# Performance work log

Hardware: AMD Instinct MI355X
Metric: run time of the kernel (lower is better)

## Reference

```python
import jax, jax.numpy as jnp
import numpy as np

DIM = 1024
NUM_HEADS = 16
HEAD_DIM = DIM // NUM_HEADS
SCALE = 1.0 / HEAD_DIM  # NOTE: module uses 1/head_dim, not 1/sqrt(head_dim)


def setup_inputs() -> dict:
    key = jax.random.key(0)
    ks = jax.random.split(key, 9)
    B, S = 2, 2048
    init = lambda k, shape: jax.random.normal(k, shape, dtype=jnp.float32) * 0.02
    return {
        "x": jax.random.normal(ks[0], (B, S, DIM), dtype=jnp.float32),
        "wq": init(ks[1], (DIM, DIM)), "bq": jnp.zeros((DIM,), jnp.float32),
        "wk": init(ks[2], (DIM, DIM)), "bk": jnp.zeros((DIM,), jnp.float32),
        "wv": init(ks[3], (DIM, DIM)), "bv": jnp.zeros((DIM,), jnp.float32),
        "wo": init(ks[4], (DIM, DIM)), "bo": jnp.zeros((DIM,), jnp.float32),
    }


def _attn(x, wq, bq, wk, bk, wv, bv, wo, bo):
    B, S, D = x.shape
    H, hd = NUM_HEADS, HEAD_DIM
    # projections; weights stored as (in, out) so y = x @ w + b
    q = (x @ wq + bq).reshape(B, S, H, hd).transpose(0, 2, 1, 3)  # [B,H,S,hd]
    k = (x @ wk + bk).reshape(B, S, H, hd).transpose(0, 2, 1, 3)
    v = (x @ wv + bv).reshape(B, S, H, hd).transpose(0, 2, 1, 3)
    scores = jnp.einsum("bhqd,bhkd->bhqk", q, k) * SCALE  # [B,H,S,S]
    # Module's mask: triu(ones, diagonal=0) kept -> attends to positions j >= i
    i = jnp.arange(S)[:, None]
    j = jnp.arange(S)[None, :]
    allowed = j >= i  # [S,S]
    scores = jnp.where(allowed[None, None], scores, -jnp.inf)
    probs = jax.nn.softmax(scores, axis=-1)
    # dropout is identity in eval/reference mode
    out = jnp.einsum("bhqk,bhkd->bhqd", probs, v)  # [B,H,S,hd]
    out = out.transpose(0, 2, 1, 3).reshape(B, S, D)
    return out @ wo + bo


def reference(x, wq, bq, wk, bk, wv, bv, wo, bo):
    return _attn(x, wq, bq, wk, bk, wv, bv, wo, bo)
```

## Files before the change

kernel.cpp:

```cpp
#include <hip/hip_runtime.h>
#include <hip/hip_bf16.h>


constexpr int NH    = 16;
constexpr int HD    = 64;
constexpr int BATCH = 2;
constexpr int SEQ   = 2048;
constexpr int DIMSZ = 1024;
constexpr float SCALE = 1.0f / 64.0f;
constexpr float QSCL = SCALE * 1.44269504088896f;

typedef __attribute__((ext_vector_type(8))) short short8;
typedef __attribute__((ext_vector_type(4))) float f32x4;
typedef __attribute__((ext_vector_type(4))) unsigned short ushort4v;

__device__ inline unsigned short f2bf(float f) {
    __hip_bfloat16 h = __float2bfloat16(f);
    unsigned short u;
    __builtin_memcpy(&u, &h, 2);
    return u;
}

__device__ __forceinline__ void gload_lds16(const void* g, void* l) {
    __builtin_amdgcn_global_load_lds(
        (const __attribute__((address_space(1))) unsigned int*)g,
        (__attribute__((address_space(3))) unsigned int*)l, 16, 0, 0);
}

__global__ __launch_bounds__(256) void cvt_x(const float* __restrict__ src,
                                             unsigned short* __restrict__ dst)
{
    const int i = blockIdx.x * 256 + threadIdx.x;
    const float4* s4 = reinterpret_cast<const float4*>(src);
    const float4 a = s4[(size_t)i * 2];
    const float4 b = s4[(size_t)i * 2 + 1];
    short8 o;
    o[0] = (short)f2bf(a.x); o[1] = (short)f2bf(a.y);
    o[2] = (short)f2bf(a.z); o[3] = (short)f2bf(a.w);
    o[4] = (short)f2bf(b.x); o[5] = (short)f2bf(b.y);
    o[6] = (short)f2bf(b.z); o[7] = (short)f2bf(b.w);
    *reinterpret_cast<short8*>(&dst[(size_t)i * 8]) = o;
}

__global__ __launch_bounds__(256) void cvt_w(const float* __restrict__ wq,
                                             const float* __restrict__ wk,
                                             const float* __restrict__ wv,
                                             const float* __restrict__ wo,
                                             unsigned short* __restrict__ wt)
{
    __shared__ float tile[64][65];
    const int t = threadIdx.x;
    const float* src = (blockIdx.z == 0) ? wq : (blockIdx.z == 1) ? wk
                     : (blockIdx.z == 2) ? wv : wo;
    const int n0 = blockIdx.x * 64, k0 = blockIdx.y * 64;

#pragma unroll
    for (int r = 0; r < 64; r += 16) {
        const int row = r + (t >> 4);
        const int c4 = (t & 15) * 4;
        const float4 v = *reinterpret_cast<const float4*>(
            &src[(size_t)(k0 + row) * DIMSZ + n0 + c4]);
        tile[row][c4 + 0] = v.x;
        tile[row][c4 + 1] = v.y;
        tile[row][c4 + 2] = v.z;
        tile[row][c4 + 3] = v.w;
    }
    __syncthreads();
#pragma unroll
    for (int rr = 0; rr < 2; ++rr) {
        const int n = rr * 32 + (t >> 3);
        const int kk0 = (t & 7) * 8;
        short8 pk;
#pragma unroll
        for (int e = 0; e < 8; ++e)
            pk[e] = (short)f2bf(tile[kk0 + e][n]);
        *reinterpret_cast<short8*>(
            &wt[((size_t)blockIdx.z * DIMSZ + n0 + n) * DIMSZ + k0 + kk0]) = pk;
    }
}

template <int EPI>
__global__ __launch_bounds__(256, 2) void mfma_gemm(
    const unsigned short* __restrict__ A, const unsigned short* __restrict__ Bt,
    const float* __restrict__ b0, const float* __restrict__ b1,
    const float* __restrict__ b2,
    unsigned short* __restrict__ q_o, unsigned short* __restrict__ k_o,
    unsigned short* __restrict__ vt_o, float* __restrict__ c_out)
{
    __shared__ unsigned short As[2][128 * 64];
    __shared__ unsigned short Bs[2][128 * 64];

    const int tid = threadIdx.x;
    const int lane = tid & 63;
    const int wv_ = tid >> 6;
    const int wr = wv_ >> 1, wc = wv_ & 1;
    const int c = lane & 15, g = lane >> 4;
    const int m0 = blockIdx.y * 128;
    const int nb0 = blockIdx.x * 128;
    const int wbase = (tid & 192) * 8;
    const int lrow = tid >> 3, ld0 = (tid & 7) * 8;

    f32x4 acc[4][4];
#pragma unroll
    for (int i = 0; i < 4; ++i)
#pragma unroll
        for (int j = 0; j < 4; ++j)
            acc[i][j] = (f32x4){0.f, 0.f, 0.f, 0.f};

    auto issue = [&](unsigned short* dA, unsigned short* dB, int k0) {
#pragma unroll
        for (int it = 0; it < 4; ++it) {
            const int row = it * 32 + lrow;
            gload_lds16(&A[(size_t)(m0 + row) * DIMSZ + k0 + ld0],
                        &dA[it * 2048 + wbase]);
            gload_lds16(&Bt[(size_t)(nb0 + row) * DIMSZ + k0 + ld0],
                        &dB[it * 2048 + wbase]);
        }
    };

    auto compute = [&](const unsigned short* Ac, const unsigned short* Bc) {
#pragma unroll
        for (int kk = 0; kk < 2; ++kk) {
            short8 af[4], bfr[4];
#pragma unroll
            for (int mi = 0; mi < 4; ++mi)
                af[mi] = *reinterpret_cast<const short8*>(
                    &Ac[(wr * 64 + mi * 16 + c) * 64 + kk * 32 + g * 8]);
#pragma unroll
            for (int ni = 0; ni < 4; ++ni)
                bfr[ni] = *reinterpret_cast<const short8*>(
                    &Bc[(wc * 64 + ni * 16 + c) * 64 + kk * 32 + g * 8]);
            __builtin_amdgcn_s_setprio(1);
#pragma unroll
            for (int mi = 0; mi < 4; ++mi)
#pragma unroll
                for (int ni = 0; ni < 4; ++ni)
                    acc[mi][ni] = __builtin_amdgcn_mfma_f32_16x16x32_bf16(
                        af[mi], bfr[ni], acc[mi][ni], 0, 0, 0);
            __builtin_amdgcn_s_setprio(0);
        }
    };

    issue(As[0], Bs[0], 0);
#pragma unroll 1
    for (int kt = 0; kt < DIMSZ / 64; kt += 2) {
        __syncthreads();
        if (kt + 1 < DIMSZ / 64) issue(As[1], Bs[1], (kt + 1) * 64);
        compute(As[0], Bs[0]);
        __syncthreads();
        if (kt + 2 < DIMSZ / 64) issue(As[0], Bs[0], (kt + 2) * 64);
        compute(As[1], Bs[1]);
    }

#pragma unroll
    for (int ni = 0; ni < 4; ++ni) {
        const int n_g = nb0 + wc * 64 + ni * 16 + c;
        if (EPI == 0) {
            const int which = n_g >> 10, nn = n_g & 1023;
            const int h = nn >> 6, d = nn & 63;
            const float bias = (which == 0 ? b0 : which == 1 ? b1 : b2)[nn];
#pragma unroll
            for (int mi = 0; mi < 4; ++mi) {
                const int m_g = m0 + wr * 64 + mi * 16 + g * 4;
                const int b = m_g >> 11, s = m_g & 2047;
                if (which == 0) {
#pragma unroll
                    for (int r = 0; r < 4; ++r)
                        q_o[((size_t)(b * NH + h) * SEQ + s + r) * HD + d] =
                            f2bf((acc[mi][ni][r] + bias) * QSCL);
                } else if (which == 1) {
#pragma unroll
                    for (int r = 0; r < 4; ++r)
                        k_o[((size_t)(b * NH + h) * SEQ + s + r) * HD + d] =
                            f2bf(acc[mi][ni][r] + bias);
                } else {
                    ushort4v pk;
#pragma unroll
                    for (int r = 0; r < 4; ++r)
                        pk[r] = f2bf(acc[mi][ni][r] + bias);
                    *reinterpret_cast<ushort4v*>(
                        &vt_o[((size_t)(b * NH + h) * HD + d) * SEQ + s]) = pk;
                }
            }
        } else {
            const float bias = b0[n_g];
#pragma unroll
            for (int mi = 0; mi < 4; ++mi) {
                const int m_g = m0 + wr * 64 + mi * 16 + g * 4;
#pragma unroll
                for (int r = 0; r < 4; ++r)
                    c_out[(size_t)(m_g + r) * DIMSZ + n_g] = acc[mi][ni][r] + bias;
            }
        }
    }
}

__device__ __forceinline__ void attn_tile(
    const short8 (&qa)[2], f32x4 (&accO)[4], float (&m_run)[4], float (&l_run)[4],
    const unsigned short* Ks, const unsigned short* Vts, unsigned short* Psw,
    const int c, const int g, const int w, const bool masked)
{
    constexpr int KS = 72;
    f32x4 sf[4];
#pragma unroll
    for (int ni = 0; ni < 4; ++ni) sf[ni] = (f32x4){0.f, 0.f, 0.f, 0.f};

    __builtin_amdgcn_s_setprio(1);
#pragma unroll
    for (int kk = 0; kk < 2; ++kk)
#pragma unroll
        for (int ni = 0; ni < 4; ++ni) {
            const short8 bkf = *reinterpret_cast<const short8*>(
                &Ks[(ni * 16 + c) * KS + kk * 32 + g * 8]);
            sf[ni] = __builtin_amdgcn_mfma_f32_16x16x32_bf16(
                qa[kk], bkf, sf[ni], 0, 0, 0);
        }
    __builtin_amdgcn_s_setprio(0);

    if (masked) {
#pragma unroll
        for (int ni = 0; ni < 4; ++ni)
#pragma unroll
            for (int r = 0; r < 4; ++r)
                if (ni * 16 + c < w * 16 + g * 4 + r) sf[ni][r] = -1e30f;
    }

#pragma unroll
    for (int r = 0; r < 4; ++r) {
        float mx = fmaxf(fmaxf(sf[0][r], sf[1][r]), fmaxf(sf[2][r], sf[3][r]));
        mx = fmaxf(mx, __shfl_xor(mx, 1, 16));
        mx = fmaxf(mx, __shfl_xor(mx, 2, 16));
        mx = fmaxf(mx, __shfl_xor(mx, 4, 16));
        mx = fmaxf(mx, __shfl_xor(mx, 8, 16));
        const float newm = fmaxf(m_run[r], mx);
        const float fac = exp2f(m_run[r] - newm);
        float rs = 0.f;
#pragma unroll
        for (int ni = 0; ni < 4; ++ni) {
            const float p = exp2f(sf[ni][r] - newm);
            sf[ni][r] = p;
            rs += p;
        }
        rs += __shfl_xor(rs, 1, 16);
        rs += __shfl_xor(rs, 2, 16);
        rs += __shfl_xor(rs, 4, 16);
        rs += __shfl_xor(rs, 8, 16);
        m_run[r] = newm;
        l_run[r] = l_run[r] * fac + rs;
#pragma unroll
        for (int ni = 0; ni < 4; ++ni) accO[ni][r] *= fac;
    }

#pragma unroll
    for (int ni = 0; ni < 4; ++ni)
#pragma unroll
        for (int r = 0; r < 4; ++r)
            Psw[(g * 4 + r) * KS + ni * 16 + c] = f2bf(sf[ni][r]);

    __builtin_amdgcn_s_setprio(1);
#pragma unroll
    for (int kk = 0; kk < 2; ++kk) {
        const short8 pa = *reinterpret_cast<const short8*>(
            &Psw[c * KS + kk * 32 + g * 8]);
#pragma unroll
        for (int ni = 0; ni < 4; ++ni) {
            const short8 vb = *reinterpret_cast<const short8*>(
                &Vts[(ni * 16 + c) * KS + kk * 32 + g * 8]);
            accO[ni] = __builtin_amdgcn_mfma_f32_16x16x32_bf16(
                pa, vb, accO[ni], 0, 0, 0);
        }
    }
    __builtin_amdgcn_s_setprio(0);
}

__global__ __launch_bounds__(256, 2) void flash_mfma(
    const unsigned short* __restrict__ q, const unsigned short* __restrict__ k,
    const unsigned short* __restrict__ vt, unsigned short* __restrict__ o)
{
    constexpr int KS = 72;
    __shared__ unsigned short Ks[64 * KS];
    __shared__ unsigned short Vts[64 * KS];
    __shared__ unsigned short Ps[4][16 * KS];

    const int tid = threadIdx.x, lane = tid & 63, w = tid >> 6;
    const int c = lane & 15, g = lane >> 4;
    const int qt1 = blockIdx.x;
    const int qt2 = 31 - qt1;
    const int h = blockIdx.y, b = blockIdx.z;
    const int head = b * NH + h;
    const unsigned short* kh = k + (size_t)head * SEQ * HD;
    const unsigned short* vth = vt + (size_t)head * HD * SEQ;
    unsigned short* Psw = &Ps[w][0];

    short8 qa1[2], qa2[2];
    {
        const size_t qb1 = ((size_t)head * SEQ + qt1 * 64 + w * 16 + c) * HD;
        qa1[0] = *reinterpret_cast<const short8*>(&q[qb1 + g * 8]);
        qa1[1] = *reinterpret_cast<const short8*>(&q[qb1 + 32 + g * 8]);
        const size_t qb2 = ((size_t)head * SEQ + qt2 * 64 + w * 16 + c) * HD;
        qa2[0] = *reinterpret_cast<const short8*>(&q[qb2 + g * 8]);
        qa2[1] = *reinterpret_cast<const short8*>(&q[qb2 + 32 + g * 8]);
    }

    f32x4 acc1[4], acc2[4];
    float m1[4], l1[4], m2[4], l2[4];
#pragma unroll
    for (int i = 0; i < 4; ++i) {
        acc1[i] = (f32x4){0.f, 0.f, 0.f, 0.f};
        acc2[i] = (f32x4){0.f, 0.f, 0.f, 0.f};
        m1[i] = -1e30f; l1[i] = 0.f;
        m2[i] = -1e30f; l2[i] = 0.f;
    }

    short8 kreg[2], vreg[2];
    {
        const int j0 = qt1 * 64;
#pragma unroll
        for (int rr = 0; rr < 2; ++rr) {
            const int chunk = rr * 256 + tid;
            const int row = chunk >> 3, d0 = (chunk & 7) * 8;
            kreg[rr] = *reinterpret_cast<const short8*>(&kh[(size_t)(j0 + row) * HD + d0]);
            vreg[rr] = *reinterpret_cast<const short8*>(&vth[(size_t)row * SEQ + j0 + d0]);
        }
    }

    for (int jt = qt1; jt < SEQ / 64; ++jt) {
        __syncthreads();
#pragma unroll
        for (int rr = 0; rr < 2; ++rr) {
            const int chunk = rr * 256 + tid;
            const int row = chunk >> 3, d0 = (chunk & 7) * 8;
            *reinterpret_cast<short8*>(&Ks[row * KS + d0]) = kreg[rr];
            *reinterpret_cast<short8*>(&Vts[row * KS + d0]) = vreg[rr];
        }
        __syncthreads();
        if (jt + 1 < SEQ / 64) {
            const int j0 = (jt + 1) * 64;
#pragma unroll
            for (int rr = 0; rr < 2; ++rr) {
                const int chunk = rr * 256 + tid;
                const int row = chunk >> 3, d0 = (chunk & 7) * 8;
                kreg[rr] = *reinterpret_cast<const short8*>(&kh[(size_t)(j0 + row) * HD + d0]);
                vreg[rr] = *reinterpret_cast<const short8*>(&vth[(size_t)row * SEQ + j0 + d0]);
            }
        }

        attn_tile(qa1, acc1, m1, l1, Ks, Vts, Psw, c, g, w, jt == qt1);
        if (jt >= qt2)
            attn_tile(qa2, acc2, m2, l2, Ks, Vts, Psw, c, g, w, jt == qt2);
    }

#pragma unroll
    for (int ni = 0; ni < 4; ++ni)
#pragma unroll
        for (int r = 0; r < 4; ++r) {
            const int d = ni * 16 + c;
            const int r1 = qt1 * 64 + w * 16 + g * 4 + r;
            o[((size_t)b * SEQ + r1) * DIMSZ + h * HD + d] =
                f2bf(acc1[ni][r] / l1[r]);
            const int r2 = qt2 * 64 + w * 16 + g * 4 + r;
            o[((size_t)b * SEQ + r2) * DIMSZ + h * HD + d] =
                f2bf(acc2[ni][r] / l2[r]);
        }
}

extern "C" void kernel_launch(void* const* d_in, const int* in_sizes, int n_in,
                              void* d_out, int out_size, void* d_ws, size_t ws_size,
                              hipStream_t stream)
{
    const float* x  = (const float*)d_in[0];
    const float* wq = (const float*)d_in[1];
    const float* bq = (const float*)d_in[2];
    const float* wk = (const float*)d_in[3];
    const float* bk = (const float*)d_in[4];
    const float* wv = (const float*)d_in[5];
    const float* bv = (const float*)d_in[6];
    const float* wo = (const float*)d_in[7];
    const float* bo = (const float*)d_in[8];
    float* out = (float*)d_out;

    const size_t M4 = (size_t)4 * 1024 * 1024;
    unsigned short* p = (unsigned short*)d_ws;
    unsigned short* x_bf  = p;
    unsigned short* wt    = p + M4;
    unsigned short* q_bf  = p + 2 * M4;
    unsigned short* k_bf  = p + 3 * M4;
    unsigned short* vt_bf = p + 4 * M4;
    unsigned short* abf   = p + 5 * M4;

    cvt_x<<<2048, 256, 0, stream>>>(x, x_bf);
    cvt_w<<<dim3(16, 16, 4), 256, 0, stream>>>(wq, wk, wv, wo, wt);

    mfma_gemm<0><<<dim3(24, 32), 256, 0, stream>>>(
        x_bf, wt, bq, bk, bv, q_bf, k_bf, vt_bf, nullptr);

    flash_mfma<<<dim3(16, 16, 2), 256, 0, stream>>>(q_bf, k_bf, vt_bf, abf);

    mfma_gemm<1><<<dim3(8, 32), 256, 0, stream>>>(
        abf, wt + (size_t)3 * 1024 * 1024, bo, nullptr, nullptr,
        nullptr, nullptr, nullptr, out);
}
```

Baseline: 228.1 us.

## Compute transposed S tile to keep P in registers, drop LDS round-trip

The QK^T MFMA now computes S^T (K as A operand, Q as B), so each lane holds a full query column and the softmax reductions need only two cross-group shuffles with a scalar running max/sum per lane. P is packed to bf16 in registers with v_cvt_pk_bf16_f32 and fed directly as the A operand of the PV MFMA, removing the per-wave P scratch buffer in LDS and its store/load. The V reads are split into two 4-element loads to match the permuted k ordering, and rescale factors and normalizers are redistributed with ds_bpermute. This trades LDS traffic and shared memory for extra bpermutes and narrower V loads.

New measurement: 211.6 us. 7.2% less time.

```diff
diff --git a/kernel.cpp b/kernel.cpp
--- a/kernel.cpp
+++ b/kernel.cpp
@@ -11,6 +11,7 @@
 constexpr float QSCL = SCALE * 1.44269504088896f;
 
 typedef __attribute__((ext_vector_type(8))) short short8;
+typedef __attribute__((ext_vector_type(4))) short short4v;
 typedef __attribute__((ext_vector_type(4))) float f32x4;
 typedef __attribute__((ext_vector_type(4))) unsigned short ushort4v;
 
@@ -19,6 +20,12 @@
     unsigned short u;
     __builtin_memcpy(&u, &h, 2);
     return u;
+}
+
+__device__ __forceinline__ unsigned int cvt_pk_bf16(float lo, float hi) {
+    unsigned int r;
+    asm("v_cvt_pk_bf16_f32 %0, %1, %2" : "=v"(r) : "v"(lo), "v"(hi));
+    return r;
 }
 
 __device__ __forceinline__ void gload_lds16(const void* g, void* l) {
@@ -196,24 +203,24 @@
 }
 
 __device__ __forceinline__ void attn_tile(
-    const short8 (&qa)[2], f32x4 (&accO)[4], float (&m_run)[4], float (&l_run)[4],
-    const unsigned short* Ks, const unsigned short* Vts, unsigned short* Psw,
+    const short8 (&qa)[2], f32x4 (&accO)[4], float &m_run, float &l_run,
+    const unsigned short* Ks, const unsigned short* Vts,
     const int c, const int g, const int w, const bool masked)
 {
     constexpr int KS = 72;
-    f32x4 sf[4];
-#pragma unroll
-    for (int ni = 0; ni < 4; ++ni) sf[ni] = (f32x4){0.f, 0.f, 0.f, 0.f};
+    f32x4 st[4];
+#pragma unroll
+    for (int ni = 0; ni < 4; ++ni) st[ni] = (f32x4){0.f, 0.f, 0.f, 0.f};
 
     __builtin_amdgcn_s_setprio(1);
 #pragma unroll
     for (int kk = 0; kk < 2; ++kk)
 #pragma unroll
         for (int ni = 0; ni < 4; ++ni) {
-            const short8 bkf = *reinterpret_cast<const short8*>(
+            const short8 kf = *reinterpret_cast<const short8*>(
                 &Ks[(ni * 16 + c) * KS + kk * 32 + g * 8]);
-            sf[ni] = __builtin_amdgcn_mfma_f32_16x16x32_bf16(
-                qa[kk], bkf, sf[ni], 0, 0, 0);
+            st[ni] = __builtin_amdgcn_mfma_f32_16x16x32_bf16(
+                kf, qa[kk], st[ni], 0, 0, 0);
         }
     __builtin_amdgcn_s_setprio(0);
 
@@ -222,54 +229,64 @@
         for (int ni = 0; ni < 4; ++ni)
 #pragma unroll
             for (int r = 0; r < 4; ++r)
-                if (ni * 16 + c < w * 16 + g * 4 + r) sf[ni][r] = -1e30f;
-    }
+                if (ni * 16 + g * 4 + r < w * 16 + c) st[ni][r] = -1e30f;
+    }
+
+    float mx = -1e30f;
+#pragma unroll
+    for (int ni = 0; ni < 4; ++ni)
+        mx = fmaxf(mx, fmaxf(fmaxf(st[ni][0], st[ni][1]),
+                             fmaxf(st[ni][2], st[ni][3])));
+    mx = fmaxf(mx, __shfl_xor(mx, 16));
+    mx = fmaxf(mx, __shfl_xor(mx, 32));
+    const float newm = fmaxf(m_run, mx);
+    const float fac = exp2f(m_run - newm);
+    float rs = 0.f;
+#pragma unroll
+    for (int ni = 0; ni < 4; ++ni)
+#pragma unroll
+        for (int r = 0; r < 4; ++r) {
+            const float p = exp2f(st[ni][r] - newm);
+            st[ni][r] = p;
+            rs += p;
+        }
+    rs += __shfl_xor(rs, 16);
+    rs += __shfl_xor(rs, 32);
+    m_run = newm;
+    l_run = l_run * fac + rs;
 
 #pragma unroll
     for (int r = 0; r < 4; ++r) {
-        float mx = fmaxf(fmaxf(sf[0][r], sf[1][r]), fmaxf(sf[2][r], sf[3][r]));
-        mx = fmaxf(mx, __shfl_xor(mx, 1, 16));
-        mx = fmaxf(mx, __shfl_xor(mx, 2, 16));
-        mx = fmaxf(mx, __shfl_xor(mx, 4, 16));
-        mx = fmaxf(mx, __shfl_xor(mx, 8, 16));
-        const float newm = fmaxf(m_run[r], mx);
-        const float fac = exp2f(m_run[r] - newm);
-        float rs = 0.f;
+        const float fr = __int_as_float(__builtin_amdgcn_ds_bpermute(
+            (g * 4 + r) * 4, __float_as_int(fac)));
+#pragma unroll
+        for (int ni = 0; ni < 4; ++ni) accO[ni][r] *= fr;
+    }
+
+    short8 pa[2];
+#pragma unroll
+    for (int kk = 0; kk < 2; ++kk) {
+        union { unsigned int u[4]; short8 s; } pu;
+        pu.u[0] = cvt_pk_bf16(st[2 * kk][0], st[2 * kk][1]);
+        pu.u[1] = cvt_pk_bf16(st[2 * kk][2], st[2 * kk][3]);
+        pu.u[2] = cvt_pk_bf16(st[2 * kk + 1][0], st[2 * kk + 1][1]);
+        pu.u[3] = cvt_pk_bf16(st[2 * kk + 1][2], st[2 * kk + 1][3]);
+        pa[kk] = pu.s;
+    }
+
+    __builtin_amdgcn_s_setprio(1);
+#pragma unroll
+    for (int kk = 0; kk < 2; ++kk)
 #pragma unroll
         for (int ni = 0; ni < 4; ++ni) {
-            const float p = exp2f(sf[ni][r] - newm);
-            sf[ni][r] = p;
-            rs += p;
-        }
-        rs += __shfl_xor(rs, 1, 16);
-        rs += __shfl_xor(rs, 2, 16);
-        rs += __shfl_xor(rs, 4, 16);
-        rs += __shfl_xor(rs, 8, 16);
-        m_run[r] = newm;
-        l_run[r] = l_run[r] * fac + rs;
-#pragma unroll
-        for (int ni = 0; ni < 4; ++ni) accO[ni][r] *= fac;
-    }
-
-#pragma unroll
-    for (int ni = 0; ni < 4; ++ni)
-#pragma unroll
-        for (int r = 0; r < 4; ++r)
-            Psw[(g * 4 + r) * KS + ni * 16 + c] = f2bf(sf[ni][r]);
-
-    __builtin_amdgcn_s_setprio(1);
-#pragma unroll
-    for (int kk = 0; kk < 2; ++kk) {
-        const short8 pa = *reinterpret_cast<const short8*>(
-            &Psw[c * KS + kk * 32 + g * 8]);
-#pragma unroll
-        for (int ni = 0; ni < 4; ++ni) {
-            const short8 vb = *reinterpret_cast<const short8*>(
-                &Vts[(ni * 16 + c) * KS + kk * 32 + g * 8]);
+            union { short4v h[2]; short8 s; } vu;
+            vu.h[0] = *reinterpret_cast<const short4v*>(
+                &Vts[(ni * 16 + c) * KS + kk * 32 + g * 4]);
+            vu.h[1] = *reinterpret_cast<const short4v*>(
+                &Vts[(ni * 16 + c) * KS + kk * 32 + 16 + g * 4]);
             accO[ni] = __builtin_amdgcn_mfma_f32_16x16x32_bf16(
-                pa, vb, accO[ni], 0, 0, 0);
-        }
-    }
+                pa[kk], vu.s, accO[ni], 0, 0, 0);
+        }
     __builtin_amdgcn_s_setprio(0);
 }
 
@@ -280,7 +297,6 @@
     constexpr int KS = 72;
     __shared__ unsigned short Ks[64 * KS];
     __shared__ unsigned short Vts[64 * KS];
-    __shared__ unsigned short Ps[4][16 * KS];
 
     const int tid = threadIdx.x, lane = tid & 63, w = tid >> 6;
     const int c = lane & 15, g = lane >> 4;
@@ -290,7 +306,6 @@
     const int head = b * NH + h;
     const unsigned short* kh = k + (size_t)head * SEQ * HD;
     const unsigned short* vth = vt + (size_t)head * HD * SEQ;
-    unsigned short* Psw = &Ps[w][0];
 
     short8 qa1[2], qa2[2];
     {
@@ -303,13 +318,11 @@
     }
 
     f32x4 acc1[4], acc2[4];
-    float m1[4], l1[4], m2[4], l2[4];
+    float m1 = -1e30f, l1 = 0.f, m2 = -1e30f, l2 = 0.f;
 #pragma unroll
     for (int i = 0; i < 4; ++i) {
         acc1[i] = (f32x4){0.f, 0.f, 0.f, 0.f};
         acc2[i] = (f32x4){0.f, 0.f, 0.f, 0.f};
-        m1[i] = -1e30f; l1[i] = 0.f;
-        m2[i] = -1e30f; l2[i] = 0.f;
     }
 
     short8 kreg[2], vreg[2];
@@ -345,23 +358,29 @@
             }
         }
 
-        attn_tile(qa1, acc1, m1, l1, Ks, Vts, Psw, c, g, w, jt == qt1);
+        attn_tile(qa1, acc1, m1, l1, Ks, Vts, c, g, w, jt == qt1);
         if (jt >= qt2)
-            attn_tile(qa2, acc2, m2, l2, Ks, Vts, Psw, c, g, w, jt == qt2);
-    }
-
-#pragma unroll
-    for (int ni = 0; ni < 4; ++ni)
-#pragma unroll
-        for (int r = 0; r < 4; ++r) {
+            attn_tile(qa2, acc2, m2, l2, Ks, Vts, c, g, w, jt == qt2);
+    }
+
+#pragma unroll
+    for (int r = 0; r < 4; ++r) {
+        const float l1r = __int_as_float(__builtin_amdgcn_ds_bpermute(
+            (g * 4 + r) * 4, __float_as_int(l1)));
+        const float l2r = __int_as_float(__builtin_amdgcn_ds_bpermute(
+            (g * 4 + r) * 4, __float_as_int(l2)));
+        const float inv1 = 1.0f / l1r, inv2 = 1.0f / l2r;
+#pragma unroll
+        for (int ni = 0; ni < 4; ++ni) {
             const int d = ni * 16 + c;
             const int r1 = qt1 * 64 + w * 16 + g * 4 + r;
             o[((size_t)b * SEQ + r1) * DIMSZ + h * HD + d] =
-                f2bf(acc1[ni][r] / l1[r]);
+                f2bf(acc1[ni][r] * inv1);
             const int r2 = qt2 * 64 + w * 16 + g * 4 + r;
             o[((size_t)b * SEQ + r2) * DIMSZ + h * HD + d] =
-                f2bf(acc2[ni][r] / l2[r]);
-        }
+                f2bf(acc2[ni][r] * inv2);
+        }
+    }
 }
 
 extern "C" void kernel_launch(void* const* d_in, const int* in_sizes, int n_in,
```
